# Optimization experiments

Measured on AMD Instinct MI355X. Metric: run time of the kernel, lower is better.

Reference implementation:

```python
import jax, jax.numpy as jnp
import numpy as np
from jax import lax

B, N, C = 16, 2048, 128
NPOINT = 512
RADII = (0.1, 0.2, 0.4)
NSAMPLES = (16, 32, 48)
C_IN = C + 3          # use_xyz: relative xyz concatenated to features
C_OUT = 128
C_MID = C_OUT // 4    # mapping_func1 out channels (non-first-layer)


def fps(xyz, npoint):
    # sequential furthest point sampling; first index is 0 (matches CUDA FPS)
    b, n, _ = xyz.shape
    def step(carry, _):
        dist, last = carry
        p = xyz[jnp.arange(b), last]                    # (B,3) last selected point
        d = jnp.sum((xyz - p[:, None, :]) ** 2, -1)     # (B,N)
        dist = jnp.minimum(dist, d)
        nxt = jnp.argmax(dist, -1).astype(jnp.int32)
        return (dist, nxt), nxt
    idx0 = jnp.zeros((b,), jnp.int32)
    (_, _), rest = lax.scan(step, (jnp.full((b, n), 1e10, jnp.float32), idx0), None, length=npoint - 1)
    return jnp.concatenate([idx0[None], rest], 0).T     # (B,npoint)


def ball_query(xyz, new_xyz, radius, nsample):
    # first `nsample` in-ball indices (in original point order), pad with first hit
    n = xyz.shape[1]
    d2 = jnp.sum((new_xyz[:, :, None, :] - xyz[:, None, :, :]) ** 2, -1)  # (B,np,N)
    scores = jnp.where(d2 < radius * radius, jnp.arange(n, dtype=jnp.int32), n)
    vals = -lax.top_k(-scores, nsample)[0]               # ascending valid indices, invalid == n
    first = vals[..., :1]                                # center is always in its own ball
    return jnp.where(vals >= n, first, vals)             # (B,np,ns) int32


def gather_points(pts, idx):
    # pts (B,N,D), idx (B,np,ns) -> (B,np,ns,D)
    return jax.vmap(lambda p, i: p[i])(pts, idx)


def sa_forward(xyz, features, W1, b1, W2, b2, Wcr, bcr):
    fi = fps(xyz, NPOINT)
    new_xyz = jax.vmap(lambda p, i: p[i])(xyz, fi)       # (B,np,3)
    featT = jnp.transpose(features, (0, 2, 1))           # (B,N,C)
    outs = []
    for r, ns in zip(RADII, NSAMPLES):
        idx = ball_query(xyz, new_xyz, r, ns)
        g_xyz = gather_points(xyz, idx)                  # (B,np,ns,3) absolute neighbor coords
        rel = g_xyz - new_xyz[:, :, None, :]             # relative coords
        gf = gather_points(featT, idx)                   # (B,np,ns,C)
        x = jnp.concatenate([rel, gf], -1)               # (B,np,ns,C_in)
        dist = jnp.linalg.norm(rel, axis=-1, keepdims=True)
        ci = jnp.broadcast_to(new_xyz[:, :, None, :], g_xyz.shape)
        h10 = jnp.concatenate([dist, ci, g_xyz, rel], -1)        # relation prior (B,np,ns,10)
        h = jax.nn.relu(h10 @ W1 + b1) @ W2 + b2                 # dynamic weights (B,np,ns,C_in)
        pooled = jnp.max(jax.nn.relu(h * x), 2)                  # (B,np,C_in) max over neighbors
        outs.append(jax.nn.relu(pooled @ Wcr + bcr))             # channel raising (B,np,C_out)
    new_features = jnp.transpose(jnp.concatenate(outs, -1), (0, 2, 1))  # (B, 3*C_out, np)
    return new_xyz, new_features


def setup_inputs() -> dict:
    key = jax.random.key(0)
    ks = jax.random.split(key, 6)
    s = 0.05
    xyz = jax.random.uniform(ks[0], (B, N, 3), jnp.float32)
    features = jax.random.normal(ks[1], (B, C, N), jnp.float32)
    W1 = jax.random.normal(ks[2], (10, C_MID), jnp.float32) * s
    b1 = jnp.zeros((C_MID,), jnp.float32)
    W2 = jax.random.normal(ks[3], (C_MID, C_IN), jnp.float32) * s
    b2 = jnp.zeros((C_IN,), jnp.float32)
    Wcr = jax.random.normal(ks[4], (C_IN, C_OUT), jnp.float32) * s
    bcr = jnp.zeros((C_OUT,), jnp.float32)
    return dict(xyz=xyz, features=features, W1=W1, b1=b1, W2=W2, b2=b2, Wcr=Wcr, bcr=bcr)


def reference(xyz, features, W1, b1, W2, b2, Wcr, bcr):
    return sa_forward(xyz, features, W1, b1, W2, b2, Wcr, bcr)
```

## Files before the change

### kernel.cpp

```cpp
#include <hip/hip_runtime.h>
#include <hip/hip_bf16.h>

#define BATCH   16
#define NPTS    2048
#define NPOINT  512
#define CFEAT   128
#define CIN     131
#define CMID    32

typedef _Float16 half8 __attribute__((ext_vector_type(8)));
typedef float floatx4 __attribute__((ext_vector_type(4)));

__device__ __forceinline__ float d2_rn(float ax, float ay, float az,
                                       float bx, float by, float bz) {
  float dx = __fsub_rn(ax, bx), dy = __fsub_rn(ay, by), dz = __fsub_rn(az, bz);
  return __fadd_rn(__fadd_rn(__fmul_rn(dx, dx), __fmul_rn(dy, dy)), __fmul_rn(dz, dz));
}

__device__ __forceinline__ void wave_key_reduce(unsigned &hi, unsigned &lo) {
#define KSTEP(CTRL, RM, BM) {                                                     \
    unsigned h2 = (unsigned)__builtin_amdgcn_update_dpp((int)hi, (int)hi, CTRL,   \
                                                        RM, BM, false);           \
    unsigned l2 = (unsigned)__builtin_amdgcn_update_dpp((int)lo, (int)lo, CTRL,   \
                                                        RM, BM, false);           \
    bool g = (h2 > hi) || (h2 == hi && l2 > lo);                                  \
    hi = g ? h2 : hi; lo = g ? l2 : lo; }
  KSTEP(0x111, 0xf, 0xf)
  KSTEP(0x112, 0xf, 0xf)
  KSTEP(0x114, 0xf, 0xe)
  KSTEP(0x118, 0xf, 0xc)
  KSTEP(0x142, 0xa, 0xf)
  KSTEP(0x143, 0xc, 0xf)
#undef KSTEP
}

__global__ __launch_bounds__(256, 1) void fps_transpose_kernel(
    const float* __restrict__ xyz, const float* __restrict__ feat,
    float* __restrict__ featT, float* __restrict__ out_xyz)
{
  int t = threadIdx.x;
  if (blockIdx.x >= BATCH) {
    __shared__ float tile[32][33];
    int m  = blockIdx.x - BATCH;
    int b  = m >> 8;
    int c0 = ((m >> 6) & 3) << 5;
    int n0 = (m & 63) << 5;
    int tx = t & 31, ty = t >> 5;
    const float* src = feat  + (size_t)b * CFEAT * NPTS;
    float*       dst = featT + (size_t)b * NPTS * CFEAT;
#pragma unroll
    for (int i = 0; i < 4; ++i)
      tile[ty + 8 * i][tx] = src[(size_t)(c0 + ty + 8 * i) * NPTS + n0 + tx];
    __syncthreads();
#pragma unroll
    for (int i = 0; i < 4; ++i)
      dst[(size_t)(n0 + ty + 8 * i) * CFEAT + c0 + tx] = tile[tx][ty + 8 * i];
    return;
  }
  __shared__ float4 sp[NPTS];
  __shared__ unsigned long long skey[2][4];
  int b = blockIdx.x, lane = t & 63, wid = t >> 6;
  const float* xb = xyz + (size_t)b * NPTS * 3;
  for (int n = t; n < NPTS; n += 256) {
    const float* p = xb + n * 3;
    sp[n] = make_float4(p[0], p[1], p[2], 0.f);
  }
  __syncthreads();
  float px[8], py[8], pz[8], d[8];
#pragma unroll
  for (int i = 0; i < 8; ++i) {
    float4 q = sp[(i << 8) + t];
    px[i] = q.x; py[i] = q.y; pz[i] = q.z;
    d[i] = 1e10f;
  }
  float cx, cy, cz;
  { float4 q = sp[0]; cx = q.x; cy = q.y; cz = q.z; }
  if (t == 0) {
    float* o = out_xyz + (size_t)b * NPOINT * 3;
    o[0] = cx; o[1] = cy; o[2] = cz;
  }
#pragma unroll 1
  for (int step = 1; step < NPOINT; ++step) {
    unsigned long long bk = 0ull;
#pragma unroll
    for (int i = 0; i < 8; ++i) {
      float dd = d2_rn(px[i], py[i], pz[i], cx, cy, cz);
      float nd = fminf(d[i], dd);
      d[i] = nd;
      unsigned long long key = ((unsigned long long)__float_as_uint(nd) << 32)
                             | (unsigned)~((i << 8) + t);
      bk = key > bk ? key : bk;
    }
    unsigned khi = (unsigned)(bk >> 32), klo = (unsigned)bk;
    wave_key_reduce(khi, klo);
    int p = step & 1;
    if (lane == 63)
      skey[p][wid] = ((unsigned long long)khi << 32) | (unsigned long long)klo;
    __syncthreads();
    unsigned long long k0 = skey[p][0], k1 = skey[p][1];
    unsigned long long k2 = skey[p][2], k3 = skey[p][3];
    unsigned long long ka = k0 > k1 ? k0 : k1;
    unsigned long long kb = k2 > k3 ? k2 : k3;
    unsigned long long km = ka > kb ? ka : kb;
    int last = (int)(~(unsigned)(km & 0xFFFFFFFFull)) & (NPTS - 1);
    float4 q = sp[last];
    cx = q.x; cy = q.y; cz = q.z;
    if (t == 0) {
      float* o = out_xyz + ((size_t)b * NPOINT + step) * 3;
      o[0] = cx; o[1] = cy; o[2] = cz;
    }
  }
}

__global__ __launch_bounds__(256) void center_kernel(
    const float* __restrict__ xyz, const float* __restrict__ featT,
    const float* __restrict__ W1, const float* __restrict__ b1,
    const float* __restrict__ W2, const float* __restrict__ b2,
    const float* __restrict__ Wcr, const float* __restrict__ bcr,
    const float* __restrict__ new_xyz, float* __restrict__ out_feat)
{
  int j = blockIdx.x, b = blockIdx.y, t = threadIdx.x;
  int wid = t >> 6, lane = t & 63;
  int quad = lane >> 4, col = lane & 15;
  __shared__ _Float16 sW2T[144][40];
  __shared__ _Float16 sH1T[96][40];
  __shared__ float sRel[96][4];
  __shared__ int   sIdx[96];
  __shared__ int   lI0[4][16], lI1[4][32], lI2[4][48];
  __shared__ int   lC[4][3];
  __shared__ float sPool[3][132];

  for (int i = t; i < 144 * 32; i += 256) {
    int m = i >> 5, k = i & 31;
    float v = (m < CIN) ? W2[k * CIN + m] : 0.f;
    sW2T[m][k] = (_Float16)v;
  }
  float cx = new_xyz[((size_t)b * NPOINT + j) * 3 + 0];
  float cy = new_xyz[((size_t)b * NPOINT + j) * 3 + 1];
  float cz = new_xyz[((size_t)b * NPOINT + j) * 3 + 2];
  {
    const float* xb = xyz + (size_t)b * NPTS * 3;
    unsigned long long lt = (1ull << lane) - 1ull;
    int c0 = 0, c1 = 0, c2 = 0;
    for (int it = 0; it < 8; ++it) {
      int n = (wid << 9) + (it << 6) + lane;
      float qx = xb[n * 3 + 0], qy = xb[n * 3 + 1], qz = xb[n * 3 + 2];
      float d2 = d2_rn(cx, cy, cz, qx, qy, qz);
      bool i0 = d2 < 0.01f, i1 = d2 < 0.04f, i2 = d2 < 0.16f;
      unsigned long long m0 = __ballot(i0), m1 = __ballot(i1), m2 = __ballot(i2);
      if (i0) { int p = c0 + __popcll(m0 & lt); if (p < 16) lI0[wid][p] = n; }
      if (i1) { int p = c1 + __popcll(m1 & lt); if (p < 32) lI1[wid][p] = n; }
      if (i2) { int p = c2 + __popcll(m2 & lt); if (p < 48) lI2[wid][p] = n; }
      c0 += __popcll(m0); c1 += __popcll(m1); c2 += __popcll(m2);
    }
    if (lane == 0) { lC[wid][0] = c0; lC[wid][1] = c1; lC[wid][2] = c2; }
  }
  __syncthreads();

  if (t < 96) {
    int rad = (t < 16) ? 0 : ((t < 48) ? 1 : 2);
    int g = t - ((rad == 0) ? 0 : ((rad == 1) ? 16 : 48));
    int q0 = lC[0][rad], q1 = lC[1][rad], q2 = lC[2][rad], q3 = lC[3][rad];
    const int* L0 = (rad == 0) ? lI0[0] : (rad == 1) ? lI1[0] : lI2[0];
    const int* L1 = (rad == 0) ? lI0[1] : (rad == 1) ? lI1[1] : lI2[1];
    const int* L2 = (rad == 0) ? lI0[2] : (rad == 1) ? lI1[2] : lI2[2];
    const int* L3 = (rad == 0) ? lI0[3] : (rad == 1) ? lI1[3] : lI2[3];
    int idx = -1, gg = g;
    if (gg < q0) idx = L0[gg]; else { gg -= q0;
    if (gg < q1) idx = L1[gg]; else { gg -= q1;
    if (gg < q2) idx = L2[gg]; else { gg -= q2;
    if (gg < q3) idx = L3[gg]; } } }
    if (idx < 0)
      idx = (q0 > 0) ? L0[0] : (q1 > 0) ? L1[0] : (q2 > 0) ? L2[0] : L3[0];
    sIdx[t] = idx;

    const float* pp = xyz + ((size_t)b * NPTS + (size_t)idx) * 3;
    float ppx = pp[0], ppy = pp[1], ppz = pp[2];
    float rx = __fsub_rn(ppx, cx), ry = __fsub_rn(ppy, cy), rz = __fsub_rn(ppz, cz);
    float dist = sqrtf(__fadd_rn(__fadd_rn(__fmul_rn(rx, rx), __fmul_rn(ry, ry)),
                                 __fmul_rn(rz, rz)));
    sRel[t][0] = rx; sRel[t][1] = ry; sRel[t][2] = rz; sRel[t][3] = 0.f;
    float h10[10] = {dist, cx, cy, cz, ppx, ppy, ppz, rx, ry, rz};
    _Float16 h1h[CMID];
#pragma unroll
    for (int k = 0; k < CMID; ++k) {
      float a = b1[k];
#pragma unroll
      for (int i = 0; i < 10; ++i) a = fmaf(h10[i], W1[i * CMID + k], a);
      h1h[k] = (_Float16)fmaxf(a, 0.f);
    }
    uint4* dstv = (uint4*)&sH1T[t][0];
    const uint4* srcv = (const uint4*)h1h;
#pragma unroll
    for (int q = 0; q < 4; ++q) dstv[q] = srcv[q];
  }
  __syncthreads();

  const float* ftb = featT + (size_t)b * NPTS * CFEAT;
#pragma unroll 1
  for (int nt = wid; nt < 9; nt += 4) {
    int c = (nt << 4) + col;
    half8 Bv = *(const half8*)&sW2T[c][quad << 3];
    float b2c = (c < CIN) ? b2[c] : 0.f;
    float sm0 = 0.f, sm1 = 0.f, sm2 = 0.f;
#pragma unroll
    for (int mt = 0; mt < 6; ++mt) {
      half8 A = *(const half8*)&sH1T[(mt << 4) + col][quad << 3];
      floatx4 acc = {0.f, 0.f, 0.f, 0.f};
      acc = __builtin_amdgcn_mfma_f32_16x16x32_f16(A, Bv, acc, 0, 0, 0);
#pragma unroll
      for (int r = 0; r < 4; ++r) {
        int sm = (mt << 4) + (quad << 2) + r;
        float x;
        if (c < 3)        x = sRel[sm][c];
        else if (c < CIN) x = ftb[(size_t)sIdx[sm] * CFEAT + (c - 3)];
        else              x = 0.f;
        float h2 = __fadd_rn(acc[r], b2c);
        float v = fmaxf(__fmul_rn(h2, x), 0.f);
        if (mt == 0)      sm0 = fmaxf(sm0, v);
        else if (mt < 3)  sm1 = fmaxf(sm1, v);
        else              sm2 = fmaxf(sm2, v);
      }
    }
    sm0 = fmaxf(sm0, __shfl_xor(sm0, 16)); sm0 = fmaxf(sm0, __shfl_xor(sm0, 32));
    sm1 = fmaxf(sm1, __shfl_xor(sm1, 16)); sm1 = fmaxf(sm1, __shfl_xor(sm1, 32));
    sm2 = fmaxf(sm2, __shfl_xor(sm2, 16)); sm2 = fmaxf(sm2, __shfl_xor(sm2, 32));
    if (quad == 0 && c < CIN) {
      sPool[0][c] = sm0; sPool[1][c] = sm1; sPool[2][c] = sm2;
    }
  }
  __syncthreads();

  if (t < CFEAT) {
    float s0 = bcr[t], s1 = s0, s2 = s0;
#pragma unroll 4
    for (int k = 0; k < CIN; ++k) {
      float w = Wcr[k * CFEAT + t];
      s0 = fmaf(sPool[0][k], w, s0);
      s1 = fmaf(sPool[1][k], w, s1);
      s2 = fmaf(sPool[2][k], w, s2);
    }
    float* ob = out_feat + (size_t)b * 384 * NPOINT + j;
    ob[(size_t)(0 * CFEAT + t) * NPOINT] = fmaxf(s0, 0.f);
    ob[(size_t)(1 * CFEAT + t) * NPOINT] = fmaxf(s1, 0.f);
    ob[(size_t)(2 * CFEAT + t) * NPOINT] = fmaxf(s2, 0.f);
  }
}

extern "C" void kernel_launch(void* const* d_in, const int* in_sizes, int n_in,
                              void* d_out, int out_size, void* d_ws, size_t ws_size,
                              hipStream_t stream) {
  const float* xyz  = (const float*)d_in[0];
  const float* feat = (const float*)d_in[1];
  const float* W1   = (const float*)d_in[2];
  const float* b1   = (const float*)d_in[3];
  const float* W2   = (const float*)d_in[4];
  const float* b2   = (const float*)d_in[5];
  const float* Wcr  = (const float*)d_in[6];
  const float* bcr  = (const float*)d_in[7];
  float* out_xyz  = (float*)d_out;
  float* out_feat = out_xyz + (size_t)BATCH * NPOINT * 3;
  float* featT    = (float*)d_ws;

  fps_transpose_kernel<<<BATCH + BATCH * 256, 256, 0, stream>>>(xyz, feat, featT, out_xyz);
  center_kernel<<<dim3(NPOINT, BATCH), 256, 0, stream>>>(
      xyz, featT, W1, b1, W2, b2, Wcr, bcr, (const float*)d_out, out_feat);
}
```

Before: 580.6 us.

## Shorten FPS critical path by carrying winner coordinates through reduction

The FPS loop now tracks the per-thread best as a float/index pair instead of 64-bit keys. The winning lane of each wave publishes its point's coordinates alongside the key, so the next center comes straight from the cross-wave reduction rather than an extra LDS lookup of the whole point cloud. Selected points are buffered in shared memory and written out once at the end. The center kernel also swaps its grid axes so blocks with neighboring ids cover different batches, stages W2 with a per-thread column loop, and caches b2 in shared memory.

```diff
diff --git a/kernel.cpp b/kernel.cpp
--- a/kernel.cpp
+++ b/kernel.cpp
@@ -57,59 +57,67 @@
       dst[(size_t)(n0 + ty + 8 * i) * CFEAT + c0 + tx] = tile[tx][ty + 8 * i];
     return;
   }
-  __shared__ float4 sp[NPTS];
-  __shared__ unsigned long long skey[2][4];
+  __shared__ __align__(16) float scoord[NPOINT * 3];
+  __shared__ __align__(16) unsigned skhi[2][4], sklo[2][4];
+  __shared__ __align__(16) float sxw[2][4], syw[2][4], szw[2][4];
   int b = blockIdx.x, lane = t & 63, wid = t >> 6;
+  (void)lane;
   const float* xb = xyz + (size_t)b * NPTS * 3;
-  for (int n = t; n < NPTS; n += 256) {
-    const float* p = xb + n * 3;
-    sp[n] = make_float4(p[0], p[1], p[2], 0.f);
-  }
-  __syncthreads();
   float px[8], py[8], pz[8], d[8];
 #pragma unroll
   for (int i = 0; i < 8; ++i) {
-    float4 q = sp[(i << 8) + t];
-    px[i] = q.x; py[i] = q.y; pz[i] = q.z;
+    int n = (i << 8) + t;
+    px[i] = xb[n * 3 + 0]; py[i] = xb[n * 3 + 1]; pz[i] = xb[n * 3 + 2];
     d[i] = 1e10f;
   }
-  float cx, cy, cz;
-  { float4 q = sp[0]; cx = q.x; cy = q.y; cz = q.z; }
-  if (t == 0) {
-    float* o = out_xyz + (size_t)b * NPOINT * 3;
-    o[0] = cx; o[1] = cy; o[2] = cz;
-  }
+  float cx = xb[0], cy = xb[1], cz = xb[2];
+  if (t == 0) { scoord[0] = cx; scoord[1] = cy; scoord[2] = cz; }
 #pragma unroll 1
   for (int step = 1; step < NPOINT; ++step) {
-    unsigned long long bk = 0ull;
+    float bv = -1.f; int bn = 0;
 #pragma unroll
     for (int i = 0; i < 8; ++i) {
       float dd = d2_rn(px[i], py[i], pz[i], cx, cy, cz);
       float nd = fminf(d[i], dd);
       d[i] = nd;
-      unsigned long long key = ((unsigned long long)__float_as_uint(nd) << 32)
-                             | (unsigned)~((i << 8) + t);
-      bk = key > bk ? key : bk;
-    }
-    unsigned khi = (unsigned)(bk >> 32), klo = (unsigned)bk;
-    wave_key_reduce(khi, klo);
+      if (nd > bv) { bv = nd; bn = (i << 8) + t; }
+    }
+    unsigned ohi = __float_as_uint(bv), olo = ~(unsigned)bn;
+    unsigned rhi = ohi, rlo = olo;
+    wave_key_reduce(rhi, rlo);
+    unsigned whi = (unsigned)__builtin_amdgcn_readlane((int)rhi, 63);
+    unsigned wlo = (unsigned)__builtin_amdgcn_readlane((int)rlo, 63);
     int p = step & 1;
-    if (lane == 63)
-      skey[p][wid] = ((unsigned long long)khi << 32) | (unsigned long long)klo;
+    if (ohi == whi && olo == wlo) {
+      int i = ((int)(~wlo)) >> 8;
+      float ox = px[0], oy = py[0], oz = pz[0];
+#pragma unroll
+      for (int k = 1; k < 8; ++k)
+        if (i == k) { ox = px[k]; oy = py[k]; oz = pz[k]; }
+      skhi[p][wid] = whi; sklo[p][wid] = wlo;
+      sxw[p][wid] = ox;  syw[p][wid] = oy;  szw[p][wid] = oz;
+    }
     __syncthreads();
-    unsigned long long k0 = skey[p][0], k1 = skey[p][1];
-    unsigned long long k2 = skey[p][2], k3 = skey[p][3];
-    unsigned long long ka = k0 > k1 ? k0 : k1;
-    unsigned long long kb = k2 > k3 ? k2 : k3;
-    unsigned long long km = ka > kb ? ka : kb;
-    int last = (int)(~(unsigned)(km & 0xFFFFFFFFull)) & (NPTS - 1);
-    float4 q = sp[last];
-    cx = q.x; cy = q.y; cz = q.z;
+    uint4  KH = *(const uint4*)skhi[p];
+    uint4  KL = *(const uint4*)sklo[p];
+    float4 XW = *(const float4*)sxw[p];
+    float4 YW = *(const float4*)syw[p];
+    float4 ZW = *(const float4*)szw[p];
+    bool gA = (KH.y > KH.x) || (KH.y == KH.x && KL.y > KL.x);
+    unsigned hA = gA ? KH.y : KH.x, lA = gA ? KL.y : KL.x;
+    float xA = gA ? XW.y : XW.x, yA = gA ? YW.y : YW.x, zA = gA ? ZW.y : ZW.x;
+    bool gB = (KH.w > KH.z) || (KH.w == KH.z && KL.w > KL.z);
+    unsigned hB = gB ? KH.w : KH.z, lB = gB ? KL.w : KL.z;
+    float xB = gB ? XW.w : XW.z, yB = gB ? YW.w : YW.z, zB = gB ? ZW.w : ZW.z;
+    bool gF = (hB > hA) || (hB == hA && lB > lA);
+    cx = gF ? xB : xA; cy = gF ? yB : yA; cz = gF ? zB : zA;
     if (t == 0) {
-      float* o = out_xyz + ((size_t)b * NPOINT + step) * 3;
-      o[0] = cx; o[1] = cy; o[2] = cz;
-    }
-  }
+      scoord[step * 3 + 0] = cx; scoord[step * 3 + 1] = cy; scoord[step * 3 + 2] = cz;
+    }
+  }
+  __syncthreads();
+  float* ob = out_xyz + (size_t)b * NPOINT * 3;
+  for (int i = t; i < NPOINT * 3; i += 256) ob[i] = scoord[i];
 }
 
 __global__ __launch_bounds__(256) void center_kernel(
@@ -119,21 +127,27 @@
     const float* __restrict__ Wcr, const float* __restrict__ bcr,
     const float* __restrict__ new_xyz, float* __restrict__ out_feat)
 {
-  int j = blockIdx.x, b = blockIdx.y, t = threadIdx.x;
+  int b = blockIdx.x, j = blockIdx.y, t = threadIdx.x;
   int wid = t >> 6, lane = t & 63;
   int quad = lane >> 4, col = lane & 15;
   __shared__ _Float16 sW2T[144][40];
   __shared__ _Float16 sH1T[96][40];
+  __shared__ float sB2[144];
   __shared__ float sRel[96][4];
   __shared__ int   sIdx[96];
   __shared__ int   lI0[4][16], lI1[4][32], lI2[4][48];
   __shared__ int   lC[4][3];
   __shared__ float sPool[3][132];
 
-  for (int i = t; i < 144 * 32; i += 256) {
-    int m = i >> 5, k = i & 31;
-    float v = (m < CIN) ? W2[k * CIN + m] : 0.f;
-    sW2T[m][k] = (_Float16)v;
+  {
+    bool act = t < 144;
+    float v;
+#pragma unroll 4
+    for (int k = 0; k < 32; ++k) {
+      v = (t < CIN) ? W2[k * CIN + t] : 0.f;
+      if (act) sW2T[t][k] = (_Float16)v;
+    }
+    if (t < 144) sB2[t] = (t < CIN) ? b2[t] : 0.f;
   }
   float cx = new_xyz[((size_t)b * NPOINT + j) * 3 + 0];
   float cy = new_xyz[((size_t)b * NPOINT + j) * 3 + 1];
@@ -201,7 +215,7 @@
   for (int nt = wid; nt < 9; nt += 4) {
     int c = (nt << 4) + col;
     half8 Bv = *(const half8*)&sW2T[c][quad << 3];
-    float b2c = (c < CIN) ? b2[c] : 0.f;
+    float b2c = sB2[c];
     float sm0 = 0.f, sm1 = 0.f, sm2 = 0.f;
 #pragma unroll
     for (int mt = 0; mt < 6; ++mt) {
@@ -263,6 +277,6 @@
   float* featT    = (float*)d_ws;
 
   fps_transpose_kernel<<<BATCH + BATCH * 256, 256, 0, stream>>>(xyz, feat, featT, out_xyz);
-  center_kernel<<<dim3(NPOINT, BATCH), 256, 0, stream>>>(
+  center_kernel<<<dim3(BATCH, NPOINT), 256, 0, stream>>>(
       xyz, featT, W1, b1, W2, b2, Wcr, bcr, (const float*)d_out, out_feat);
 }
```

After: 689.7 us. +18.8%, slower.

## Shrink center kernel to 128 threads, swap grid order, buffer FPS coords in LDS

Applied to the files above, without the earlier changes.

The center kernel now runs with 128 threads (2 waves) per block instead of 256, and each wave scans two of the four point ranges in the ball query and takes more MFMA column tiles. The grid is reordered so that batch is the fast dimension. W2 is transposed per column and b2 is staged into shared memory. FPS keeps the selected coordinates in LDS and writes them out once at the end instead of storing from thread 0 on every step. The aims are lower per-block overhead, less redundant weight staging, and removing serialized global stores from the FPS loop, at the cost of less parallelism inside each block.

```diff
diff --git a/kernel.cpp b/kernel.cpp
--- a/kernel.cpp
+++ b/kernel.cpp
@@ -59,6 +59,7 @@
   }
   __shared__ float4 sp[NPTS];
   __shared__ unsigned long long skey[2][4];
+  __shared__ float scoord[NPOINT * 3];
   int b = blockIdx.x, lane = t & 63, wid = t >> 6;
   const float* xb = xyz + (size_t)b * NPTS * 3;
   for (int n = t; n < NPTS; n += 256) {
@@ -75,10 +76,7 @@
   }
   float cx, cy, cz;
   { float4 q = sp[0]; cx = q.x; cy = q.y; cz = q.z; }
-  if (t == 0) {
-    float* o = out_xyz + (size_t)b * NPOINT * 3;
-    o[0] = cx; o[1] = cy; o[2] = cz;
-  }
+  if (t == 0) { scoord[0] = cx; scoord[1] = cy; scoord[2] = cz; }
 #pragma unroll 1
   for (int step = 1; step < NPOINT; ++step) {
     unsigned long long bk = 0ull;
@@ -106,34 +104,39 @@
     float4 q = sp[last];
     cx = q.x; cy = q.y; cz = q.z;
     if (t == 0) {
-      float* o = out_xyz + ((size_t)b * NPOINT + step) * 3;
-      o[0] = cx; o[1] = cy; o[2] = cz;
-    }
-  }
-}
-
-__global__ __launch_bounds__(256) void center_kernel(
+      scoord[step * 3 + 0] = cx; scoord[step * 3 + 1] = cy; scoord[step * 3 + 2] = cz;
+    }
+  }
+  __syncthreads();
+  float* ob = out_xyz + (size_t)b * NPOINT * 3;
+  for (int i = t; i < NPOINT * 3; i += 256) ob[i] = scoord[i];
+}
+
+__global__ __launch_bounds__(128) void center_kernel(
     const float* __restrict__ xyz, const float* __restrict__ featT,
     const float* __restrict__ W1, const float* __restrict__ b1,
     const float* __restrict__ W2, const float* __restrict__ b2,
     const float* __restrict__ Wcr, const float* __restrict__ bcr,
     const float* __restrict__ new_xyz, float* __restrict__ out_feat)
 {
-  int j = blockIdx.x, b = blockIdx.y, t = threadIdx.x;
+  int b = blockIdx.x, j = blockIdx.y, t = threadIdx.x;
   int wid = t >> 6, lane = t & 63;
   int quad = lane >> 4, col = lane & 15;
   __shared__ _Float16 sW2T[144][40];
   __shared__ _Float16 sH1T[96][40];
+  __shared__ float sB2[144];
   __shared__ float sRel[96][4];
   __shared__ int   sIdx[96];
   __shared__ int   lI0[4][16], lI1[4][32], lI2[4][48];
   __shared__ int   lC[4][3];
   __shared__ float sPool[3][132];
 
-  for (int i = t; i < 144 * 32; i += 256) {
-    int m = i >> 5, k = i & 31;
-    float v = (m < CIN) ? W2[k * CIN + m] : 0.f;
-    sW2T[m][k] = (_Float16)v;
+  for (int c = t; c < 144; c += 128) {
+    bool in = c < CIN;
+#pragma unroll 4
+    for (int k = 0; k < 32; ++k)
+      sW2T[c][k] = (_Float16)(in ? W2[k * CIN + c] : 0.f);
+    sB2[c] = in ? b2[c] : 0.f;
   }
   float cx = new_xyz[((size_t)b * NPOINT + j) * 3 + 0];
   float cy = new_xyz[((size_t)b * NPOINT + j) * 3 + 1];
@@ -141,19 +144,24 @@
   {
     const float* xb = xyz + (size_t)b * NPTS * 3;
     unsigned long long lt = (1ull << lane) - 1ull;
-    int c0 = 0, c1 = 0, c2 = 0;
-    for (int it = 0; it < 8; ++it) {
-      int n = (wid << 9) + (it << 6) + lane;
-      float qx = xb[n * 3 + 0], qy = xb[n * 3 + 1], qz = xb[n * 3 + 2];
-      float d2 = d2_rn(cx, cy, cz, qx, qy, qz);
-      bool i0 = d2 < 0.01f, i1 = d2 < 0.04f, i2 = d2 < 0.16f;
-      unsigned long long m0 = __ballot(i0), m1 = __ballot(i1), m2 = __ballot(i2);
-      if (i0) { int p = c0 + __popcll(m0 & lt); if (p < 16) lI0[wid][p] = n; }
-      if (i1) { int p = c1 + __popcll(m1 & lt); if (p < 32) lI1[wid][p] = n; }
-      if (i2) { int p = c2 + __popcll(m2 & lt); if (p < 48) lI2[wid][p] = n; }
-      c0 += __popcll(m0); c1 += __popcll(m1); c2 += __popcll(m2);
-    }
-    if (lane == 0) { lC[wid][0] = c0; lC[wid][1] = c1; lC[wid][2] = c2; }
+#pragma unroll 1
+    for (int half = 0; half < 2; ++half) {
+      int rng = (wid << 1) + half;
+      int c0 = 0, c1 = 0, c2 = 0;
+#pragma unroll 1
+      for (int it = 0; it < 8; ++it) {
+        int n = (rng << 9) + (it << 6) + lane;
+        float qx = xb[n * 3 + 0], qy = xb[n * 3 + 1], qz = xb[n * 3 + 2];
+        float d2 = d2_rn(cx, cy, cz, qx, qy, qz);
+        bool i0 = d2 < 0.01f, i1 = d2 < 0.04f, i2 = d2 < 0.16f;
+        unsigned long long m0 = __ballot(i0), m1 = __ballot(i1), m2 = __ballot(i2);
+        if (i0) { int p = c0 + __popcll(m0 & lt); if (p < 16) lI0[rng][p] = n; }
+        if (i1) { int p = c1 + __popcll(m1 & lt); if (p < 32) lI1[rng][p] = n; }
+        if (i2) { int p = c2 + __popcll(m2 & lt); if (p < 48) lI2[rng][p] = n; }
+        c0 += __popcll(m0); c1 += __popcll(m1); c2 += __popcll(m2);
+      }
+      if (lane == 0) { lC[rng][0] = c0; lC[rng][1] = c1; lC[rng][2] = c2; }
+    }
   }
   __syncthreads();
 
@@ -197,11 +205,10 @@
   __syncthreads();
 
   const float* ftb = featT + (size_t)b * NPTS * CFEAT;
-#pragma unroll 1
-  for (int nt = wid; nt < 9; nt += 4) {
+  for (int nt = wid; nt < 9; nt += 2) {
     int c = (nt << 4) + col;
     half8 Bv = *(const half8*)&sW2T[c][quad << 3];
-    float b2c = (c < CIN) ? b2[c] : 0.f;
+    float b2c = sB2[c];
     float sm0 = 0.f, sm1 = 0.f, sm2 = 0.f;
 #pragma unroll
     for (int mt = 0; mt < 6; ++mt) {
@@ -231,7 +238,7 @@
   }
   __syncthreads();
 
-  if (t < CFEAT) {
+  {
     float s0 = bcr[t], s1 = s0, s2 = s0;
 #pragma unroll 4
     for (int k = 0; k < CIN; ++k) {
@@ -263,6 +270,6 @@
   float* featT    = (float*)d_ws;
 
   fps_transpose_kernel<<<BATCH + BATCH * 256, 256, 0, stream>>>(xyz, feat, featT, out_xyz);
-  center_kernel<<<dim3(NPOINT, BATCH), 256, 0, stream>>>(
+  center_kernel<<<dim3(BATCH, NPOINT), 128, 0, stream>>>(
       xyz, featT, W1, b1, W2, b2, Wcr, bcr, (const float*)d_out, out_feat);
 }
```

Result: faster. 564.3 us (-2.8%).
